# Kernel tuning notes

Hardware: AMD Instinct MI355X
Metric: run time of the kernel (lower is better)

Reference implementation:

```python
import jax, jax.numpy as jnp
import numpy as np


def _gcn_conv(x, W, b, src, dst, dinv):
    # h = x @ W, then symmetric-normalized aggregation with self-loops (PyG GCNConv)
    n = x.shape[0]
    h = x @ W  # [N, H]
    norm_e = dinv[src] * dinv[dst]  # [E]
    msgs = h[src] * norm_e[:, None]  # [E, H] gathered+scaled messages
    agg = jax.ops.segment_sum(msgs, dst, num_segments=n)
    # self-loop contribution: norm = dinv[i]^2
    agg = agg + h * (dinv * dinv)[:, None]
    return agg + b


def setup_inputs() -> dict:
    key = jax.random.key(0)
    k1, k2, k3, k4, k5 = jax.random.split(key, 5)
    N, E, C_in, H = 50000, 800000, 256, 128
    x = jax.random.normal(k1, (N, C_in), dtype=jnp.float32)
    edge_index = jax.random.randint(k2, (2, E), 0, N, dtype=jnp.int32)
    s = 1.0 / np.sqrt(C_in)
    W1 = jax.random.uniform(k3, (C_in, H), jnp.float32, -s, s)
    b1 = jnp.zeros((H,), jnp.float32)
    s2 = 1.0 / np.sqrt(H)
    W_mu = jax.random.uniform(k4, (H, H), jnp.float32, -s2, s2)
    b_mu = jnp.zeros((H,), jnp.float32)
    W_ls = jax.random.uniform(k5, (H, H), jnp.float32, -s2, s2)
    b_ls = jnp.zeros((H,), jnp.float32)
    return {"x": x, "edge_index": edge_index, "W1": W1, "b1": b1,
            "W_mu": W_mu, "b_mu": b_mu, "W_ls": W_ls, "b_ls": b_ls}


def reference(x, edge_index, W1, b1, W_mu, b_mu, W_ls, b_ls):
    n = x.shape[0]
    src, dst = edge_index[0], edge_index[1]
    # degree with self-loops (count incoming edges at target + 1)
    deg = jax.ops.segment_sum(jnp.ones_like(dst, dtype=x.dtype), dst, num_segments=n) + 1.0
    dinv = jax.lax.rsqrt(deg)
    h = jax.nn.relu(_gcn_conv(x, W1, b1, src, dst, dinv))
    mu = _gcn_conv(h, W_mu, b_mu, src, dst, dinv)
    logstd = _gcn_conv(h, W_ls, b_ls, src, dst, dinv)
    return mu, logstd
```

## Files before the change

### kernel.cpp

```cpp
#include <hip/hip_runtime.h>
#include <hip/hip_bf16.h>
#include <cstdint>

#define HFEAT 128
#define CIN   256

typedef unsigned int  uint;
typedef unsigned short ushort;
typedef short bf16x8 __attribute__((ext_vector_type(8)));
typedef float f32x4  __attribute__((ext_vector_type(4)));

__device__ inline float bflo(uint u){ return __uint_as_float(u << 16); }
__device__ inline float bfhi(uint u){ return __uint_as_float(u & 0xffff0000u); }
__device__ inline uint  f2bf(float f){
  union { __hip_bfloat16 b; ushort u; } cvt;
  cvt.b = __float2bfloat16(f);
  return (uint)cvt.u;
}


__global__ void k_zero_i32(int* __restrict__ p, int n){
  int i = blockIdx.x*blockDim.x + threadIdx.x;
  if (i < n) p[i] = 0;
}

__global__ void k_count(const int* __restrict__ dst, int E, int* __restrict__ counts){
  int e = blockIdx.x*blockDim.x + threadIdx.x;
  if (e < E) atomicAdd(&counts[dst[e]], 1);
}

__global__ void k_dinv(const int* __restrict__ counts, int n, float* __restrict__ dinv){
  int i = blockIdx.x*blockDim.x + threadIdx.x;
  if (i < n) dinv[i] = rsqrtf((float)counts[i] + 1.0f);
}

__global__ void k_scan1(const int* __restrict__ counts, int n,
                        int* __restrict__ excl, int* __restrict__ bsum){
  __shared__ int sm[1024];
  int t = threadIdx.x;
  int i = blockIdx.x*1024 + t;
  int v = (i < n) ? counts[i] : 0;
  sm[t] = v;
  __syncthreads();
  for (int off = 1; off < 1024; off <<= 1){
    int add = (t >= off) ? sm[t-off] : 0;
    __syncthreads();
    sm[t] += add;
    __syncthreads();
  }
  if (i < n) excl[i] = sm[t] - v;
  if (t == 1023) bsum[blockIdx.x] = sm[t];
}

__global__ void k_scan2(int* __restrict__ bsum, int nb){
  if (threadIdx.x == 0 && blockIdx.x == 0){
    int run = 0;
    for (int b = 0; b < nb; b++){ int v = bsum[b]; bsum[b] = run; run += v; }
  }
}

__global__ void k_scan3(const int* __restrict__ bsum, int n, int E,
                        int* __restrict__ rowoff, int* __restrict__ cursor){
  int i = blockIdx.x*blockDim.x + threadIdx.x;
  if (i < n){
    int v = rowoff[i] + bsum[blockIdx.x];
    rowoff[i] = v;
    cursor[i] = v;
  }
  if (i == 0) rowoff[n] = E;
}

__global__ void k_fill(const int* __restrict__ src, const int* __restrict__ dst, int E,
                       const float* __restrict__ dinv, int* __restrict__ cursor,
                       int2* __restrict__ csr){
  int e = blockIdx.x*blockDim.x + threadIdx.x;
  if (e < E){
    int s = src[e], d = dst[e];
    int pos = atomicAdd(&cursor[d], 1);
    csr[pos] = make_int2(s, __float_as_int(dinv[s]*dinv[d]));
  }
}


template<int K>
__global__ void k_cvt_wt(const float* __restrict__ W, ushort* __restrict__ Wt){
  int n = blockIdx.x;
  int k = threadIdx.x;
  Wt[n * K + k] = (ushort)f2bf(W[(size_t)k * HFEAT + n]);
}


template<int K, bool IN_BF16, bool BIAS, bool OUT_BF16>
__global__ void __launch_bounds__(256) k_gemm_mfma(const void* __restrict__ Ain,
                                                   const ushort* __restrict__ Wta,
                                                   const ushort* __restrict__ Wtb,
                                                   const float* __restrict__ ba,
                                                   const float* __restrict__ bb,
                                                   void* __restrict__ outa,
                                                   void* __restrict__ outb,
                                                   int n){
  __shared__ ushort Abuf[64][72];
  __shared__ ushort Bbuf[128][72];

  const ushort* Wt   = (blockIdx.y == 0) ? Wta : Wtb;
  const float*  bias = (blockIdx.y == 0) ? ba  : bb;
  void*         outv = (blockIdx.y == 0) ? outa : outb;

  const int tid  = threadIdx.x;
  const int w    = tid >> 6;
  const int l    = tid & 63;
  const int l15  = l & 15;
  const int lhi  = l >> 4;
  const int row0 = blockIdx.x * 64;

  const int ar = tid >> 2;
  const int aq = tid & 3;
  int arow = row0 + ar; if (arow >= n) arow = n - 1;

  f32x4 acc[8];
  #pragma unroll
  for (int t = 0; t < 8; t++) acc[t] = (f32x4){0.f, 0.f, 0.f, 0.f};

  const int NT = K / 64;
  #pragma unroll
  for (int kt = 0; kt < NT; ++kt){
    if (IN_BF16){
      const ushort* ap = (const ushort*)Ain + (size_t)arow * K + aq * 16 + kt * 64;
      uint4 v0 = *(const uint4*)(ap);
      uint4 v1 = *(const uint4*)(ap + 8);
      *(uint4*)&Abuf[ar][aq * 16]     = v0;
      *(uint4*)&Abuf[ar][aq * 16 + 8] = v1;
    } else {
      const float* p = (const float*)Ain + (size_t)arow * K + aq * 16 + kt * 64;
      float4 v0 = *(const float4*)(p);
      float4 v1 = *(const float4*)(p + 4);
      float4 v2 = *(const float4*)(p + 8);
      float4 v3 = *(const float4*)(p + 12);
      uint4 pa, pb;
      pa.x = f2bf(v0.x) | (f2bf(v0.y) << 16);
      pa.y = f2bf(v0.z) | (f2bf(v0.w) << 16);
      pa.z = f2bf(v1.x) | (f2bf(v1.y) << 16);
      pa.w = f2bf(v1.z) | (f2bf(v1.w) << 16);
      pb.x = f2bf(v2.x) | (f2bf(v2.y) << 16);
      pb.y = f2bf(v2.z) | (f2bf(v2.w) << 16);
      pb.z = f2bf(v3.x) | (f2bf(v3.y) << 16);
      pb.w = f2bf(v3.z) | (f2bf(v3.w) << 16);
      *(uint4*)&Abuf[ar][aq * 16]     = pa;
      *(uint4*)&Abuf[ar][aq * 16 + 8] = pb;
    }
    #pragma unroll
    for (int j = 0; j < 4; ++j){
      int flat = tid + 256 * j;
      int bn = flat >> 3;
      int bk = (flat & 7) * 8;
      uint4 v = *(const uint4*)(Wt + (size_t)bn * K + kt * 64 + bk);
      *(uint4*)&Bbuf[bn][bk] = v;
    }
    __syncthreads();

    #pragma unroll
    for (int ks = 0; ks < 2; ++ks){
      const int ko = ks * 32 + lhi * 8;
      bf16x8 af = *(bf16x8*)&Abuf[16 * w + l15][ko];
      #pragma unroll
      for (int nt = 0; nt < 8; ++nt){
        bf16x8 bf = *(bf16x8*)&Bbuf[nt * 16 + l15][ko];
        acc[nt] = __builtin_amdgcn_mfma_f32_16x16x32_bf16(af, bf, acc[nt], 0, 0, 0);
      }
    }
    __syncthreads();
  }

  float bv[8];
  #pragma unroll
  for (int nt = 0; nt < 8; ++nt) bv[nt] = BIAS ? bias[nt * 16 + l15] : 0.f;

  #pragma unroll
  for (int j = 0; j < 4; ++j){
    int r = row0 + 16 * w + lhi * 4 + j;
    if (r < n){
      if (OUT_BF16){
        ushort* orow = (ushort*)outv + (size_t)r * HFEAT + l15;
        #pragma unroll
        for (int nt = 0; nt < 8; ++nt)
          orow[nt * 16] = (ushort)f2bf(acc[nt][j] + bv[nt]);
      } else {
        float* orow = (float*)outv + (size_t)r * HFEAT + l15;
        #pragma unroll
        for (int nt = 0; nt < 8; ++nt)
          orow[nt * 16] = acc[nt][j] + bv[nt];
      }
    }
  }
}


template<int RELU, bool OUT_BF16>
__global__ void __launch_bounds__(256) k_agg(const ushort* __restrict__ in,
                                             const float* __restrict__ bias,
                                             const int* __restrict__ rowoff,
                                             const int2* __restrict__ csr,
                                             const float* __restrict__ dinv,
                                             void* __restrict__ out, int n){
  int gid  = blockIdx.x*blockDim.x + threadIdx.x;
  int node = gid >> 6;
  int lane = gid & 63;
  if (node >= n) return;
  const int w  = lane >> 4;
  const int q  = lane & 15;
  const int f0 = q * 8;

  float acc[8] = {0,0,0,0,0,0,0,0};

  const int e0 = rowoff[node], e1 = rowoff[node+1];
  #pragma unroll 2
  for (int e = e0 + w; e < e1; e += 4){
    int2 c = csr[e];
    uint4 v = *(const uint4*)(in + ((size_t)c.x << 7) + f0);
    float wv = __int_as_float(c.y);
    acc[0] = fmaf(bflo(v.x), wv, acc[0]);
    acc[1] = fmaf(bfhi(v.x), wv, acc[1]);
    acc[2] = fmaf(bflo(v.y), wv, acc[2]);
    acc[3] = fmaf(bfhi(v.y), wv, acc[3]);
    acc[4] = fmaf(bflo(v.z), wv, acc[4]);
    acc[5] = fmaf(bfhi(v.z), wv, acc[5]);
    acc[6] = fmaf(bflo(v.w), wv, acc[6]);
    acc[7] = fmaf(bfhi(v.w), wv, acc[7]);
  }
  if (w == 0){
    float di = dinv[node];
    float sw = di * di;
    uint4 v = *(const uint4*)(in + ((size_t)node << 7) + f0);
    acc[0] = fmaf(bflo(v.x), sw, acc[0]);
    acc[1] = fmaf(bfhi(v.x), sw, acc[1]);
    acc[2] = fmaf(bflo(v.y), sw, acc[2]);
    acc[3] = fmaf(bfhi(v.y), sw, acc[3]);
    acc[4] = fmaf(bflo(v.z), sw, acc[4]);
    acc[5] = fmaf(bfhi(v.z), sw, acc[5]);
    acc[6] = fmaf(bflo(v.w), sw, acc[6]);
    acc[7] = fmaf(bfhi(v.w), sw, acc[7]);
  }
  #pragma unroll
  for (int j = 0; j < 8; j++){
    acc[j] += __shfl_xor(acc[j], 16);
    acc[j] += __shfl_xor(acc[j], 32);
  }

  if (RELU){
    float4 b0 = *(const float4*)&bias[f0];
    float4 b1 = *(const float4*)&bias[f0 + 4];
    acc[0] = fmaxf(acc[0] + b0.x, 0.f);
    acc[1] = fmaxf(acc[1] + b0.y, 0.f);
    acc[2] = fmaxf(acc[2] + b0.z, 0.f);
    acc[3] = fmaxf(acc[3] + b0.w, 0.f);
    acc[4] = fmaxf(acc[4] + b1.x, 0.f);
    acc[5] = fmaxf(acc[5] + b1.y, 0.f);
    acc[6] = fmaxf(acc[6] + b1.z, 0.f);
    acc[7] = fmaxf(acc[7] + b1.w, 0.f);
  }

  if (w == 0){
    if (OUT_BF16){
      uint4 p;
      p.x = f2bf(acc[0]) | (f2bf(acc[1]) << 16);
      p.y = f2bf(acc[2]) | (f2bf(acc[3]) << 16);
      p.z = f2bf(acc[4]) | (f2bf(acc[5]) << 16);
      p.w = f2bf(acc[6]) | (f2bf(acc[7]) << 16);
      *(uint4*)((ushort*)out + ((size_t)node << 7) + f0) = p;
    } else {
      float* o = (float*)out + ((size_t)node << 7) + f0;
      *(float4*)o       = make_float4(acc[0], acc[1], acc[2], acc[3]);
      *(float4*)(o + 4) = make_float4(acc[4], acc[5], acc[6], acc[7]);
    }
  }
}


extern "C" void kernel_launch(void* const* d_in, const int* in_sizes, int n_in,
                              void* d_out, int out_size, void* d_ws, size_t ws_size,
                              hipStream_t stream){
  const float* x   = (const float*)d_in[0];
  const int*   ei  = (const int*)  d_in[1];
  const float* W1  = (const float*)d_in[2];
  const float* b1  = (const float*)d_in[3];
  const float* Wmu = (const float*)d_in[4];
  const float* bmu = (const float*)d_in[5];
  const float* Wls = (const float*)d_in[6];
  const float* bls = (const float*)d_in[7];
  int N = in_sizes[0] / CIN;
  int E = in_sizes[1] / 2;
  const int* src = ei;
  const int* dst = ei + E;
  float* out = (float*)d_out;

  char* w = (char*)d_ws;
  auto alloc = [&](size_t bytes)->char*{
    char* p = w; w += (bytes + 255) & ~(size_t)255; return p;
  };
  ushort* hW1b  = (ushort*)alloc((size_t)N*HFEAT*2);
  ushort* hb    = (ushort*)alloc((size_t)N*HFEAT*2);
  ushort* gb    = (ushort*)alloc((size_t)N*HFEAT*2);
  ushort* W1bt  = (ushort*)alloc((size_t)HFEAT*CIN*2);
  ushort* Wmut  = (ushort*)alloc((size_t)HFEAT*HFEAT*2);
  ushort* Wlst  = (ushort*)alloc((size_t)HFEAT*HFEAT*2);
  int*   counts = (int*)   alloc((size_t)N*4);
  float* dinv   = (float*) alloc((size_t)N*4);
  int*   rowoff = (int*)   alloc(((size_t)N+1)*4);
  int*   cursor = (int*)   alloc((size_t)N*4);
  int*   bsum   = (int*)   alloc(256*4);
  int2*  csr    = (int2*)  alloc((size_t)E*8);

  int nbN  = (N + 255) / 256;
  int nbE  = (E + 255) / 256;
  int nbS  = (N + 1023) / 1024;
  int nbG  = (N + 63) / 64;

  k_zero_i32<<<nbN, 256, 0, stream>>>(counts, N);
  k_count   <<<nbE, 256, 0, stream>>>(dst, E, counts);
  k_dinv    <<<nbN, 256, 0, stream>>>(counts, N, dinv);
  k_scan1   <<<nbS, 1024, 0, stream>>>(counts, N, rowoff, bsum);
  k_scan2   <<<1, 64, 0, stream>>>(bsum, nbS);
  k_scan3   <<<nbS, 1024, 0, stream>>>(bsum, N, E, rowoff, cursor);
  k_fill    <<<nbE, 256, 0, stream>>>(src, dst, E, dinv, cursor, csr);
  k_cvt_wt<CIN>  <<<HFEAT, CIN,   0, stream>>>(W1,  W1bt);
  k_cvt_wt<HFEAT><<<HFEAT, HFEAT, 0, stream>>>(Wmu, Wmut);
  k_cvt_wt<HFEAT><<<HFEAT, HFEAT, 0, stream>>>(Wls, Wlst);

  k_gemm_mfma<CIN, false, false, true><<<dim3(nbG, 1), 256, 0, stream>>>(
      x, W1bt, W1bt, nullptr, nullptr, hW1b, hW1b, N);
  int aggBlocks = (int)(((size_t)N*64 + 255) / 256);
  k_agg<1, true><<<aggBlocks, 256, 0, stream>>>(hW1b, b1, rowoff, csr, dinv, hb, N);
  k_agg<0, true><<<aggBlocks, 256, 0, stream>>>(hb, nullptr, rowoff, csr, dinv, gb, N);
  k_gemm_mfma<HFEAT, true, true, false><<<dim3(nbG, 2), 256, 0, stream>>>(
      gb, Wmut, Wlst, bmu, bls, out, out + (size_t)N*HFEAT, N);
}
```

Baseline: 298.6 us.

## Factor symmetric normalization into row scaling and shrink CSR to source indices

Rewrites the GCN normalization so features are pre-scaled by dinv[src] (in the GEMM epilogue or the previous aggregation) and post-scaled by dinv[dst], which lets the CSR store only 4-byte source indices instead of index plus weight pairs. The aggregation loop becomes plain adds, cutting edge-list traffic in half. It also merges the dinv computation into the scan, replaces the zero kernel with a memset and fuses the three weight conversions into one launch, reducing the number of launches. The extra bf16 rounding of pre-scaled intermediates slightly changes numerics.

```diff
diff --git a/kernel.cpp b/kernel.cpp
--- a/kernel.cpp
+++ b/kernel.cpp
@@ -19,27 +19,19 @@
 }
 
 
-__global__ void k_zero_i32(int* __restrict__ p, int n){
-  int i = blockIdx.x*blockDim.x + threadIdx.x;
-  if (i < n) p[i] = 0;
-}
-
 __global__ void k_count(const int* __restrict__ dst, int E, int* __restrict__ counts){
   int e = blockIdx.x*blockDim.x + threadIdx.x;
   if (e < E) atomicAdd(&counts[dst[e]], 1);
 }
 
-__global__ void k_dinv(const int* __restrict__ counts, int n, float* __restrict__ dinv){
-  int i = blockIdx.x*blockDim.x + threadIdx.x;
-  if (i < n) dinv[i] = rsqrtf((float)counts[i] + 1.0f);
-}
-
 __global__ void k_scan1(const int* __restrict__ counts, int n,
-                        int* __restrict__ excl, int* __restrict__ bsum){
+                        int* __restrict__ excl, int* __restrict__ bsum,
+                        float* __restrict__ dinv){
   __shared__ int sm[1024];
   int t = threadIdx.x;
   int i = blockIdx.x*1024 + t;
   int v = (i < n) ? counts[i] : 0;
+  if (i < n) dinv[i] = rsqrtf((float)v + 1.0f);
   sm[t] = v;
   __syncthreads();
   for (int off = 1; off < 1024; off <<= 1){
@@ -71,31 +63,38 @@
 }
 
 __global__ void k_fill(const int* __restrict__ src, const int* __restrict__ dst, int E,
-                       const float* __restrict__ dinv, int* __restrict__ cursor,
-                       int2* __restrict__ csr){
+                       int* __restrict__ cursor, int* __restrict__ csr4){
   int e = blockIdx.x*blockDim.x + threadIdx.x;
   if (e < E){
-    int s = src[e], d = dst[e];
-    int pos = atomicAdd(&cursor[d], 1);
-    csr[pos] = make_int2(s, __float_as_int(dinv[s]*dinv[d]));
-  }
-}
-
-
-template<int K>
-__global__ void k_cvt_wt(const float* __restrict__ W, ushort* __restrict__ Wt){
-  int n = blockIdx.x;
-  int k = threadIdx.x;
-  Wt[n * K + k] = (ushort)f2bf(W[(size_t)k * HFEAT + n]);
-}
-
-
-template<int K, bool IN_BF16, bool BIAS, bool OUT_BF16>
+    int pos = atomicAdd(&cursor[dst[e]], 1);
+    csr4[pos] = src[e];
+  }
+}
+
+
+__global__ void k_cvt_all(const float* __restrict__ W1,  const float* __restrict__ Wmu,
+                          const float* __restrict__ Wls, ushort* __restrict__ W1t,
+                          ushort* __restrict__ Wmut, ushort* __restrict__ Wlst){
+  int b = blockIdx.x, t = threadIdx.x;
+  if (b < 128){
+    W1t[b * CIN + t] = (ushort)f2bf(W1[(size_t)t * HFEAT + b]);
+  } else if (b < 256){
+    int nn = b - 128;
+    if (t < HFEAT) Wmut[nn * HFEAT + t] = (ushort)f2bf(Wmu[(size_t)t * HFEAT + nn]);
+  } else {
+    int nn = b - 256;
+    if (t < HFEAT) Wlst[nn * HFEAT + t] = (ushort)f2bf(Wls[(size_t)t * HFEAT + nn]);
+  }
+}
+
+
+template<int K, bool IN_BF16, bool BIAS, bool OUT_BF16, bool SCALE_DINV>
 __global__ void __launch_bounds__(256) k_gemm_mfma(const void* __restrict__ Ain,
                                                    const ushort* __restrict__ Wta,
                                                    const ushort* __restrict__ Wtb,
                                                    const float* __restrict__ ba,
                                                    const float* __restrict__ bb,
+                                                   const float* __restrict__ dinv,
                                                    void* __restrict__ outa,
                                                    void* __restrict__ outb,
                                                    int n){
@@ -179,11 +178,12 @@
   for (int j = 0; j < 4; ++j){
     int r = row0 + 16 * w + lhi * 4 + j;
     if (r < n){
+      float sc = SCALE_DINV ? dinv[r] : 1.f;
       if (OUT_BF16){
         ushort* orow = (ushort*)outv + (size_t)r * HFEAT + l15;
         #pragma unroll
         for (int nt = 0; nt < 8; ++nt)
-          orow[nt * 16] = (ushort)f2bf(acc[nt][j] + bv[nt]);
+          orow[nt * 16] = (ushort)f2bf((acc[nt][j] + bv[nt]) * sc);
       } else {
         float* orow = (float*)outv + (size_t)r * HFEAT + l15;
         #pragma unroll
@@ -195,13 +195,13 @@
 }
 
 
-template<int RELU, bool OUT_BF16>
+template<int RELU>
 __global__ void __launch_bounds__(256) k_agg(const ushort* __restrict__ in,
                                              const float* __restrict__ bias,
                                              const int* __restrict__ rowoff,
-                                             const int2* __restrict__ csr,
+                                             const int* __restrict__ csr4,
                                              const float* __restrict__ dinv,
-                                             void* __restrict__ out, int n){
+                                             ushort* __restrict__ out, int n){
   int gid  = blockIdx.x*blockDim.x + threadIdx.x;
   int node = gid >> 6;
   int lane = gid & 63;
@@ -215,30 +215,19 @@
   const int e0 = rowoff[node], e1 = rowoff[node+1];
   #pragma unroll 2
   for (int e = e0 + w; e < e1; e += 4){
-    int2 c = csr[e];
-    uint4 v = *(const uint4*)(in + ((size_t)c.x << 7) + f0);
-    float wv = __int_as_float(c.y);
-    acc[0] = fmaf(bflo(v.x), wv, acc[0]);
-    acc[1] = fmaf(bfhi(v.x), wv, acc[1]);
-    acc[2] = fmaf(bflo(v.y), wv, acc[2]);
-    acc[3] = fmaf(bfhi(v.y), wv, acc[3]);
-    acc[4] = fmaf(bflo(v.z), wv, acc[4]);
-    acc[5] = fmaf(bfhi(v.z), wv, acc[5]);
-    acc[6] = fmaf(bflo(v.w), wv, acc[6]);
-    acc[7] = fmaf(bfhi(v.w), wv, acc[7]);
+    int s = csr4[e];
+    uint4 v = *(const uint4*)(in + ((size_t)s << 7) + f0);
+    acc[0] += bflo(v.x); acc[1] += bfhi(v.x);
+    acc[2] += bflo(v.y); acc[3] += bfhi(v.y);
+    acc[4] += bflo(v.z); acc[5] += bfhi(v.z);
+    acc[6] += bflo(v.w); acc[7] += bfhi(v.w);
   }
   if (w == 0){
-    float di = dinv[node];
-    float sw = di * di;
     uint4 v = *(const uint4*)(in + ((size_t)node << 7) + f0);
-    acc[0] = fmaf(bflo(v.x), sw, acc[0]);
-    acc[1] = fmaf(bfhi(v.x), sw, acc[1]);
-    acc[2] = fmaf(bflo(v.y), sw, acc[2]);
-    acc[3] = fmaf(bfhi(v.y), sw, acc[3]);
-    acc[4] = fmaf(bflo(v.z), sw, acc[4]);
-    acc[5] = fmaf(bfhi(v.z), sw, acc[5]);
-    acc[6] = fmaf(bflo(v.w), sw, acc[6]);
-    acc[7] = fmaf(bfhi(v.w), sw, acc[7]);
+    acc[0] += bflo(v.x); acc[1] += bfhi(v.x);
+    acc[2] += bflo(v.y); acc[3] += bfhi(v.y);
+    acc[4] += bflo(v.z); acc[5] += bfhi(v.z);
+    acc[6] += bflo(v.w); acc[7] += bfhi(v.w);
   }
   #pragma unroll
   for (int j = 0; j < 8; j++){
@@ -246,32 +235,31 @@
     acc[j] += __shfl_xor(acc[j], 32);
   }
 
-  if (RELU){
-    float4 b0 = *(const float4*)&bias[f0];
-    float4 b1 = *(const float4*)&bias[f0 + 4];
-    acc[0] = fmaxf(acc[0] + b0.x, 0.f);
-    acc[1] = fmaxf(acc[1] + b0.y, 0.f);
-    acc[2] = fmaxf(acc[2] + b0.z, 0.f);
-    acc[3] = fmaxf(acc[3] + b0.w, 0.f);
-    acc[4] = fmaxf(acc[4] + b1.x, 0.f);
-    acc[5] = fmaxf(acc[5] + b1.y, 0.f);
-    acc[6] = fmaxf(acc[6] + b1.z, 0.f);
-    acc[7] = fmaxf(acc[7] + b1.w, 0.f);
-  }
-
   if (w == 0){
-    if (OUT_BF16){
-      uint4 p;
-      p.x = f2bf(acc[0]) | (f2bf(acc[1]) << 16);
-      p.y = f2bf(acc[2]) | (f2bf(acc[3]) << 16);
-      p.z = f2bf(acc[4]) | (f2bf(acc[5]) << 16);
-      p.w = f2bf(acc[6]) | (f2bf(acc[7]) << 16);
-      *(uint4*)((ushort*)out + ((size_t)node << 7) + f0) = p;
+    float di = dinv[node];
+    uint4 p;
+    if (RELU){
+      float4 b0 = *(const float4*)&bias[f0];
+      float4 b1 = *(const float4*)&bias[f0 + 4];
+      float r0 = fmaxf(fmaf(acc[0], di, b0.x), 0.f) * di;
+      float r1 = fmaxf(fmaf(acc[1], di, b0.y), 0.f) * di;
+      float r2 = fmaxf(fmaf(acc[2], di, b0.z), 0.f) * di;
+      float r3 = fmaxf(fmaf(acc[3], di, b0.w), 0.f) * di;
+      float r4 = fmaxf(fmaf(acc[4], di, b1.x), 0.f) * di;
+      float r5 = fmaxf(fmaf(acc[5], di, b1.y), 0.f) * di;
+      float r6 = fmaxf(fmaf(acc[6], di, b1.z), 0.f) * di;
+      float r7 = fmaxf(fmaf(acc[7], di, b1.w), 0.f) * di;
+      p.x = f2bf(r0) | (f2bf(r1) << 16);
+      p.y = f2bf(r2) | (f2bf(r3) << 16);
+      p.z = f2bf(r4) | (f2bf(r5) << 16);
+      p.w = f2bf(r6) | (f2bf(r7) << 16);
     } else {
-      float* o = (float*)out + ((size_t)node << 7) + f0;
-      *(float4*)o       = make_float4(acc[0], acc[1], acc[2], acc[3]);
-      *(float4*)(o + 4) = make_float4(acc[4], acc[5], acc[6], acc[7]);
-    }
+      p.x = f2bf(acc[0] * di) | (f2bf(acc[1] * di) << 16);
+      p.y = f2bf(acc[2] * di) | (f2bf(acc[3] * di) << 16);
+      p.z = f2bf(acc[4] * di) | (f2bf(acc[5] * di) << 16);
+      p.w = f2bf(acc[6] * di) | (f2bf(acc[7] * di) << 16);
+    }
+    *(uint4*)(out + ((size_t)node << 7) + f0) = p;
   }
 }
 
@@ -297,8 +285,8 @@
   auto alloc = [&](size_t bytes)->char*{
     char* p = w; w += (bytes + 255) & ~(size_t)255; return p;
   };
-  ushort* hW1b  = (ushort*)alloc((size_t)N*HFEAT*2);
-  ushort* hb    = (ushort*)alloc((size_t)N*HFEAT*2);
+  ushort* t1    = (ushort*)alloc((size_t)N*HFEAT*2);
+  ushort* t2    = (ushort*)alloc((size_t)N*HFEAT*2);
   ushort* gb    = (ushort*)alloc((size_t)N*HFEAT*2);
   ushort* W1bt  = (ushort*)alloc((size_t)HFEAT*CIN*2);
   ushort* Wmut  = (ushort*)alloc((size_t)HFEAT*HFEAT*2);
@@ -308,29 +296,25 @@
   int*   rowoff = (int*)   alloc(((size_t)N+1)*4);
   int*   cursor = (int*)   alloc((size_t)N*4);
   int*   bsum   = (int*)   alloc(256*4);
-  int2*  csr    = (int2*)  alloc((size_t)E*8);
-
-  int nbN  = (N + 255) / 256;
+  int*   csr4   = (int*)   alloc((size_t)E*4);
+
   int nbE  = (E + 255) / 256;
   int nbS  = (N + 1023) / 1024;
   int nbG  = (N + 63) / 64;
 
-  k_zero_i32<<<nbN, 256, 0, stream>>>(counts, N);
+  hipMemsetAsync(counts, 0, (size_t)N*4, stream);
   k_count   <<<nbE, 256, 0, stream>>>(dst, E, counts);
-  k_dinv    <<<nbN, 256, 0, stream>>>(counts, N, dinv);
-  k_scan1   <<<nbS, 1024, 0, stream>>>(counts, N, rowoff, bsum);
+  k_scan1   <<<nbS, 1024, 0, stream>>>(counts, N, rowoff, bsum, dinv);
   k_scan2   <<<1, 64, 0, stream>>>(bsum, nbS);
   k_scan3   <<<nbS, 1024, 0, stream>>>(bsum, N, E, rowoff, cursor);
-  k_fill    <<<nbE, 256, 0, stream>>>(src, dst, E, dinv, cursor, csr);
-  k_cvt_wt<CIN>  <<<HFEAT, CIN,   0, stream>>>(W1,  W1bt);
-  k_cvt_wt<HFEAT><<<HFEAT, HFEAT, 0, stream>>>(Wmu, Wmut);
-  k_cvt_wt<HFEAT><<<HFEAT, HFEAT, 0, stream>>>(Wls, Wlst);
-
-  k_gemm_mfma<CIN, false, false, true><<<dim3(nbG, 1), 256, 0, stream>>>(
-      x, W1bt, W1bt, nullptr, nullptr, hW1b, hW1b, N);
+  k_fill    <<<nbE, 256, 0, stream>>>(src, dst, E, cursor, csr4);
+  k_cvt_all <<<384, 256, 0, stream>>>(W1, Wmu, Wls, W1bt, Wmut, Wlst);
+
+  k_gemm_mfma<CIN, false, false, true, true><<<dim3(nbG, 1), 256, 0, stream>>>(
+      x, W1bt, W1bt, nullptr, nullptr, dinv, t1, t1, N);
   int aggBlocks = (int)(((size_t)N*64 + 255) / 256);
-  k_agg<1, true><<<aggBlocks, 256, 0, stream>>>(hW1b, b1, rowoff, csr, dinv, hb, N);
-  k_agg<0, true><<<aggBlocks, 256, 0, stream>>>(hb, nullptr, rowoff, csr, dinv, gb, N);
-  k_gemm_mfma<HFEAT, true, true, false><<<dim3(nbG, 2), 256, 0, stream>>>(
-      gb, Wmut, Wlst, bmu, bls, out, out + (size_t)N*HFEAT, N);
-}
+  k_agg<1><<<aggBlocks, 256, 0, stream>>>(t1, b1, rowoff, csr4, dinv, t2, N);
+  k_agg<0><<<aggBlocks, 256, 0, stream>>>(t2, nullptr, rowoff, csr4, dinv, gb, N);
+  k_gemm_mfma<HFEAT, true, true, false, false><<<dim3(nbG, 2), 256, 0, stream>>>(
+      gb, Wmut, Wlst, bmu, bls, nullptr, out, out + (size_t)N*HFEAT, N);
+}
```

After: 295.3 us. About the same (-1.1%).
